# Kernel optimization log

Hardware: AMD Instinct MI355X
Metric: run time of the kernel (lower is better)

## Reference

```python
import jax, jax.numpy as jnp
import numpy as np

D_MODEL = 1024
HEAD_DIM = 256
MEMORY_SIZE = 64
SPARSITY_RATIO = 0.1
NEG_INF = -1.0e9


def setup_inputs() -> dict:
    key = jax.random.key(0)
    ks = jax.random.split(key, 16)
    s = lambda fan_in: 1.0 / np.sqrt(fan_in)
    inp = {
        "x": jax.random.normal(ks[0], (2, 4096, D_MODEL), dtype=jnp.float32),
        # local attention head (qkv fused, no bias); weights stored [in, out]
        "local_qkv_w": jax.random.uniform(ks[1], (D_MODEL, 3 * HEAD_DIM), minval=-s(D_MODEL), maxval=s(D_MODEL)),
        # sparse global head
        "sparse_qkv_w": jax.random.uniform(ks[2], (D_MODEL, 3 * HEAD_DIM), minval=-s(D_MODEL), maxval=s(D_MODEL)),
        # memory head
        "memory_bank": jax.random.normal(ks[3], (MEMORY_SIZE, HEAD_DIM), dtype=jnp.float32),
        "memory_proj_w": jax.random.uniform(ks[4], (D_MODEL, HEAD_DIM), minval=-s(D_MODEL), maxval=s(D_MODEL)),
        "mem_out_w": jax.random.uniform(ks[5], (2 * HEAD_DIM, HEAD_DIM), minval=-s(2 * HEAD_DIM), maxval=s(2 * HEAD_DIM)),
        "mem_out_b": jax.random.uniform(ks[6], (HEAD_DIM,), minval=-s(2 * HEAD_DIM), maxval=s(2 * HEAD_DIM)),
        # prediction head
        "pred_in_w": jax.random.uniform(ks[7], (D_MODEL, HEAD_DIM), minval=-s(D_MODEL), maxval=s(D_MODEL)),
        "pred_in_b": jax.random.uniform(ks[8], (HEAD_DIM,), minval=-s(D_MODEL), maxval=s(D_MODEL)),
        "pred1_w": jax.random.uniform(ks[9], (HEAD_DIM, 2 * HEAD_DIM), minval=-s(HEAD_DIM), maxval=s(HEAD_DIM)),
        "pred1_b": jax.random.uniform(ks[10], (2 * HEAD_DIM,), minval=-s(HEAD_DIM), maxval=s(HEAD_DIM)),
        "pred2_w": jax.random.uniform(ks[11], (2 * HEAD_DIM, HEAD_DIM), minval=-s(2 * HEAD_DIM), maxval=s(2 * HEAD_DIM)),
        "pred2_b": jax.random.uniform(ks[12], (HEAD_DIM,), minval=-s(2 * HEAD_DIM), maxval=s(2 * HEAD_DIM)),
        # warboss output projection
        "warboss_w": jax.random.uniform(ks[13], (4 * HEAD_DIM, D_MODEL), minval=-s(4 * HEAD_DIM), maxval=s(4 * HEAD_DIM)),
        "warboss_b": jax.random.uniform(ks[14], (D_MODEL,), minval=-s(4 * HEAD_DIM), maxval=s(4 * HEAD_DIM)),
    }
    return inp


def _full_attention(x, qkv_w, scale):
    # x: [B,S,D] -> q,k,v: [B,S,H]
    qkv = x @ qkv_w
    q, k, v = jnp.split(qkv, 3, axis=-1)
    scores = jnp.einsum("bsh,bth->bst", q, k) * scale  # [B,S,S]
    probs = jax.nn.softmax(scores, axis=-1)
    return probs @ v


def _sparse_global_attention(x, qkv_w, scale):
    qkv = x @ qkv_w
    q, k, v = jnp.split(qkv, 3, axis=-1)
    scores = jnp.einsum("bsh,bth->bst", q, k) * scale  # [B,S,S]
    seq_len = x.shape[1]
    k_sparse = max(1, int(seq_len * SPARSITY_RATIO))
    topk_vals, _ = jax.lax.top_k(scores, k_sparse)
    kth = topk_vals[..., -1:]  # [B,S,1] threshold
    masked = jnp.where(scores >= kth, scores, NEG_INF)
    probs = jax.nn.softmax(masked, axis=-1)
    return probs @ v


def _memory_head(x, memory_bank, memory_proj_w, mem_out_w, mem_out_b):
    x_proj = x @ memory_proj_w  # [B,S,H]
    mem_scores = jnp.einsum("bsh,mh->bsm", x_proj, memory_bank)
    mem_weights = jax.nn.softmax(mem_scores, axis=-1)
    retrieved = jnp.einsum("bsm,mh->bsh", mem_weights, memory_bank)
    combined = jnp.concatenate([x_proj, retrieved], axis=-1)
    return combined @ mem_out_w + mem_out_b


def _prediction_head(x, pred_in_w, pred_in_b, pred1_w, pred1_b, pred2_w, pred2_b):
    h = x @ pred_in_w + pred_in_b
    h = h @ pred1_w + pred1_b
    h = jax.nn.gelu(h, approximate=False)
    return h @ pred2_w + pred2_b


def reference(x, local_qkv_w, sparse_qkv_w, memory_bank, memory_proj_w, mem_out_w, mem_out_b, pred_in_w, pred_in_b, pred1_w, pred1_b, pred2_w, pred2_b, warboss_w, warboss_b):
    scale = HEAD_DIM ** -0.5
    local_out = _full_attention(x, local_qkv_w, scale)
    sparse_out = _sparse_global_attention(x, sparse_qkv_w, scale)
    mem_out = _memory_head(x, memory_bank, memory_proj_w, mem_out_w, mem_out_b)
    pred_out = _prediction_head(x, pred_in_w, pred_in_b, pred1_w, pred1_b, pred2_w, pred2_b)
    combined = jnp.concatenate([local_out, sparse_out, mem_out, pred_out], axis=-1)
    return combined @ warboss_w + warboss_b
```

## Files before the change

### kernel.cpp

```cpp
#include <hip/hip_runtime.h>
#include <hip/hip_bf16.h>

typedef __attribute__((ext_vector_type(8))) _Float16 half8;
typedef __attribute__((ext_vector_type(4))) _Float16 half4v;
typedef __attribute__((ext_vector_type(4))) float f32x4;

__device__ __forceinline__ float wred_max(float v){
  #pragma unroll
  for (int o = 32; o; o >>= 1) v = fmaxf(v, __shfl_xor(v, o));
  return v;
}
__device__ __forceinline__ float wred_sum(float v){
  #pragma unroll
  for (int o = 32; o; o >>= 1) v += __shfl_xor(v, o);
  return v;
}
__device__ __forceinline__ unsigned short h2u(_Float16 h){
  unsigned short u;
  __builtin_memcpy(&u, &h, 2);
  return u;
}
__device__ __forceinline__ float u2hf(unsigned short u){
  _Float16 h;
  __builtin_memcpy(&h, &u, 2);
  return (float)h;
}

#define GLOAD16(GP, LP) __builtin_amdgcn_global_load_lds( \
    (const __attribute__((address_space(1))) void*)(GP),  \
    (__attribute__((address_space(3))) void*)(LP), 16, 0, 0)

template<int BM, int BN, int OUT_F16, int ACT>
__global__ __launch_bounds__(256) void gemm_ht(
    const _Float16* __restrict__ A, long saz, int lda,
    const _Float16* __restrict__ B, long sbz, int ldb,
    void* __restrict__ Cv, long scz, int ldc,
    int K, float alpha, const float* __restrict__ bias)
{
  constexpr int FM = BM / 32, FN = BN / 32;
  __shared__ __align__(16) _Float16 Asl[2][BM * 32];
  __shared__ __align__(16) _Float16 Bsl[2][BN * 32];
  const int t = threadIdx.x;
  const int wid = t >> 6, lane = t & 63;
  const int wr = wid >> 1, wc = wid & 1;
  const int lr = lane & 15, kg = lane >> 4;
  A += (long)blockIdx.z * saz;
  B += (long)blockIdx.z * sbz;
  const long row0 = (long)blockIdx.y * BM;
  const long col0 = (long)blockIdx.x * BN;

  const int arow_t = t >> 2, acol_t = (t & 3) * 8;

  auto stage = [&](int buf, int k0){
    #pragma unroll
    for (int r = 0; r < BM / 64; r++){
      const _Float16* gp = A + (row0 + r*64 + arow_t) * (long)lda + k0 + acol_t;
      GLOAD16(gp, (char*)Asl[buf] + r*4096 + wid*1024);
    }
    #pragma unroll
    for (int r = 0; r < BN / 64; r++){
      const _Float16* gp = B + (col0 + r*64 + arow_t) * (long)ldb + k0 + acol_t;
      GLOAD16(gp, (char*)Bsl[buf] + r*4096 + wid*1024);
    }
  };

  f32x4 acc[FM][FN];
  #pragma unroll
  for (int i = 0; i < FM; i++)
    #pragma unroll
    for (int j = 0; j < FN; j++)
      acc[i][j] = (f32x4){0.f, 0.f, 0.f, 0.f};

  stage(0, 0);
  __syncthreads();
  int cur = 0;
  for (int k0 = 0; k0 < K; k0 += 32){
    if (k0 + 32 < K) stage(cur ^ 1, k0 + 32);
    half8 af[FM], bfv[FN];
    #pragma unroll
    for (int i = 0; i < FM; i++)
      af[i] = *(const half8*)((const char*)Asl[cur] + (wr*(BM/2) + i*16 + lr)*64 + kg*16);
    #pragma unroll
    for (int j = 0; j < FN; j++)
      bfv[j] = *(const half8*)((const char*)Bsl[cur] + (wc*(BN/2) + j*16 + lr)*64 + kg*16);
    #pragma unroll
    for (int i = 0; i < FM; i++)
      #pragma unroll
      for (int j = 0; j < FN; j++)
        acc[i][j] = __builtin_amdgcn_mfma_f32_16x16x32_f16(af[i], bfv[j], acc[i][j], 0, 0, 0);
    __syncthreads();
    cur ^= 1;
  }

  _Float16* Ch = (_Float16*)Cv + (long)blockIdx.z * scz;
  float*    Cf = (float*)Cv    + (long)blockIdx.z * scz;
  #pragma unroll
  for (int i = 0; i < FM; i++){
    #pragma unroll
    for (int j = 0; j < FN; j++){
      #pragma unroll
      for (int q = 0; q < 4; q++){
        long rr = row0 + wr*(BM/2) + i*16 + kg*4 + q;
        long cc = col0 + wc*(BN/2) + j*16 + lr;
        float val = acc[i][j][q] * alpha;
        if (bias) val += bias[cc];
        if constexpr (ACT) val = 0.5f * val * (1.0f + erff(val * 0.70710678118654752f));
        if constexpr (OUT_F16) Ch[rr*(long)ldc + cc] = (_Float16)val;
        else                   Cf[rr*(long)ldc + cc] = val;
      }
    }
  }
}

template<int BM, int BN, int SPARSE>
__global__ __launch_bounds__(256) void gemm_pv_exp(
    const _Float16* __restrict__ A, long saz, int lda,
    const _Float16* __restrict__ B, long sbz, int ldb,
    const float4* __restrict__ mlthr,
    _Float16* __restrict__ Ph, int nsplit, int Ksplit)
{
  constexpr int FM = BM / 32, FN = BN / 32;
  __shared__ __align__(16) _Float16 Asl[2][BM * 32];
  __shared__ __align__(16) _Float16 Bsl[2][BN * 32];
  const int t = threadIdx.x;
  const int wid = t >> 6, lane = t & 63;
  const int wr = wid >> 1, wc = wid & 1;
  const int lr = lane & 15, kg = lane >> 4;
  const int z = blockIdx.z, batch = z / nsplit, split = z % nsplit;
  A += (long)batch * saz;
  B += (long)batch * sbz;
  _Float16* Pz = Ph + (size_t)z * (4096 * 256);
  const long row0 = (long)blockIdx.y * BM;
  const int Kbase = split * Ksplit;

  const long arow = row0 + (t >> 2);
  const float4 mt = mlthr[(long)batch*4096 + arow];
  const float m = mt.x, thr = mt.z;
  const _Float16* Ap = A + arow * (long)lda + Kbase + (t & 3) * 8;

  const int arow_t = t >> 2, acol_t = (t & 3) * 8;

  auto stageB = [&](int buf, int k0){
    #pragma unroll
    for (int r = 0; r < BN / 64; r++){
      const _Float16* gp = B + (r*64 + arow_t) * (long)ldb + Kbase + k0 + acol_t;
      GLOAD16(gp, (char*)Bsl[buf] + r*4096 + wid*1024);
    }
  };
  auto expw = [&](int buf, half8 ld){
    half8 st;
    #pragma unroll
    for (int e = 0; e < 8; e++){
      float v = (float)ld[e];
      float ev;
      if constexpr (SPARSE) ev = (v >= thr) ? __expf(v - m) : 0.f;
      else                  ev = __expf(v - m);
      st[e] = (_Float16)ev;
    }
    *(half8*)((char*)Asl[buf] + t*16) = st;
  };

  f32x4 acc[FM][FN];
  #pragma unroll
  for (int i = 0; i < FM; i++)
    #pragma unroll
    for (int j = 0; j < FN; j++)
      acc[i][j] = (f32x4){0.f, 0.f, 0.f, 0.f};

  stageB(0, 0);
  expw(0, *(const half8*)(Ap + 0));
  __syncthreads();
  int cur = 0;
  for (int k0 = 0; k0 < Ksplit; k0 += 32){
    const bool more = (k0 + 32 < Ksplit);
    half8 lda_next;
    if (more){
      stageB(cur ^ 1, k0 + 32);
      lda_next = *(const half8*)(Ap + k0 + 32);
    }
    half8 af[FM], bfv[FN];
    #pragma unroll
    for (int i = 0; i < FM; i++)
      af[i] = *(const half8*)((const char*)Asl[cur] + (wr*(BM/2) + i*16 + lr)*64 + kg*16);
    #pragma unroll
    for (int j = 0; j < FN; j++)
      bfv[j] = *(const half8*)((const char*)Bsl[cur] + (wc*(BN/2) + j*16 + lr)*64 + kg*16);
    #pragma unroll
    for (int i = 0; i < FM; i++)
      #pragma unroll
      for (int j = 0; j < FN; j++)
        acc[i][j] = __builtin_amdgcn_mfma_f32_16x16x32_f16(af[i], bfv[j], acc[i][j], 0, 0, 0);
    if (more) expw(cur ^ 1, lda_next);
    __syncthreads();
    cur ^= 1;
  }

  #pragma unroll
  for (int i = 0; i < FM; i++)
    #pragma unroll
    for (int j = 0; j < FN; j++)
      #pragma unroll
      for (int q = 0; q < 4; q++){
        long rr = row0 + wr*(BM/2) + i*16 + kg*4 + q;
        long cc = wc*(BN/2) + j*16 + lr;
        Pz[rr*256 + cc] = (_Float16)acc[i][j][q];
      }
}

__global__ __launch_bounds__(256) void reduce8h(const _Float16* __restrict__ Ph,
                                                const float4* __restrict__ mlthr,
                                                _Float16* __restrict__ dst, int coff, int nq){
  int i = blockIdx.x * 256 + threadIdx.x;
  if (i >= nq) return;
  int b = i >> 18;
  int r = i & 262143;
  int row = r >> 6, col4 = r & 63;
  float sx = 0.f, sy = 0.f, sz = 0.f, sw = 0.f;
  #pragma unroll
  for (int sp = 0; sp < 8; sp++){
    half4v p = *(const half4v*)(Ph + (((size_t)(b*8 + sp)*4096 + row)*256 + col4*4));
    sx += (float)p[0]; sy += (float)p[1]; sz += (float)p[2]; sw += (float)p[3];
  }
  const float inv = 1.0f / mlthr[(long)b*4096 + row].y;
  half4v o;
  o[0] = (_Float16)(sx*inv); o[1] = (_Float16)(sy*inv);
  o[2] = (_Float16)(sz*inv); o[3] = (_Float16)(sw*inv);
  *(half4v*)(dst + ((size_t)b*4096 + row)*1024 + coff + col4*4) = o;
}

__global__ __launch_bounds__(256) void cast_xh(const float* __restrict__ in,
                                               _Float16* __restrict__ out, int n8){
  int i = blockIdx.x * 256 + threadIdx.x;
  const int stride = gridDim.x * 256;
  for (; i < n8; i += stride){
    float4 a = ((const float4*)in)[2*i];
    float4 b = ((const float4*)in)[2*i + 1];
    half8 o;
    o[0]=(_Float16)a.x; o[1]=(_Float16)a.y; o[2]=(_Float16)a.z; o[3]=(_Float16)a.w;
    o[4]=(_Float16)b.x; o[5]=(_Float16)b.y; o[6]=(_Float16)b.z; o[7]=(_Float16)b.w;
    *(half8*)(out + (size_t)i*8) = o;
  }
}

__global__ __launch_bounds__(256) void transpose_cast_w(const float* __restrict__ in, int R, int C,
                                                        _Float16* __restrict__ out){
  __shared__ float tile[32][33];
  const int c0 = blockIdx.x * 32, r0 = blockIdx.y * 32;
  const int tx = threadIdx.x & 31, ty = threadIdx.x >> 5;
  #pragma unroll
  for (int i = 0; i < 32; i += 8)
    tile[ty+i][tx] = in[(size_t)(r0+ty+i)*C + c0+tx];
  __syncthreads();
  #pragma unroll
  for (int i = 0; i < 32; i += 8)
    out[(size_t)(c0+ty+i)*R + r0+tx] = (_Float16)tile[tx][ty+i];
}

__global__ __launch_bounds__(256) void transpose_h(
    const _Float16* __restrict__ in, long in_z, int ld_in,
    _Float16* __restrict__ out, long out_z, int ld_out)
{
  __shared__ _Float16 tile[32][34];
  const _Float16* ip = in + (long)blockIdx.z * in_z;
  _Float16* op = out + (long)blockIdx.z * out_z;
  const int c0 = blockIdx.x * 32, r0 = blockIdx.y * 32;
  const int tx = threadIdx.x & 31, ty = threadIdx.x >> 5;
  #pragma unroll
  for (int i = 0; i < 32; i += 8)
    tile[ty+i][tx] = ip[(long)(r0+ty+i)*ld_in + c0+tx];
  __syncthreads();
  #pragma unroll
  for (int i = 0; i < 32; i += 8)
    op[(long)(c0+ty+i)*ld_out + r0+tx] = tile[tx][ty+i];
}

__global__ __launch_bounds__(256) void rowstat_local(const _Float16* __restrict__ sc,
                                                     float4* __restrict__ mlthr){
  __shared__ float red[4], red2[4];
  const int t = threadIdx.x, lane = t & 63, wid = t >> 6;
  const _Float16* p = sc + (size_t)blockIdx.x * 4096;
  half8 a = ((const half8*)p)[t*2];
  half8 b = ((const half8*)p)[t*2 + 1];
  float v[16];
  #pragma unroll
  for (int e = 0; e < 8; e++){ v[e] = (float)a[e]; v[8+e] = (float)b[e]; }
  float m = v[0];
  #pragma unroll
  for (int e = 1; e < 16; e++) m = fmaxf(m, v[e]);
  m = wred_max(m);
  if (lane == 0) red[wid] = m;
  __syncthreads();
  m = fmaxf(fmaxf(red[0], red[1]), fmaxf(red[2], red[3]));
  float s = 0.f;
  #pragma unroll
  for (int e = 0; e < 16; e++) s += __expf(v[e] - m);
  s = wred_sum(s);
  if (lane == 0) red2[wid] = s;
  __syncthreads();
  if (t == 0){
    s = red2[0] + red2[1] + red2[2] + red2[3];
    mlthr[blockIdx.x] = make_float4(m, s, -3.0e38f, 0.f);
  }
}

__global__ __launch_bounds__(256) void rowstat_sparse(const _Float16* __restrict__ sc,
                                                      float4* __restrict__ mlthr, int ksel){
  __shared__ unsigned hist4[4][256];
  __shared__ unsigned hrev[256];
  __shared__ unsigned suf[257];
  __shared__ unsigned wtot[4];
  __shared__ int selb;
  __shared__ float red[4], red2[4];
  const int t = threadIdx.x, lane = t & 63, wid = t >> 6;
  const _Float16* p = sc + (size_t)blockIdx.x * 4096;
  half8 a = ((const half8*)p)[t*2];
  half8 b = ((const half8*)p)[t*2 + 1];
  float v[16]; unsigned kk[16];
  #pragma unroll
  for (int e = 0; e < 8; e++){
    unsigned short u0 = h2u(a[e]);
    unsigned short u1 = h2u(b[e]);
    kk[e]   = (u0 & 0x8000u) ? (unsigned)(unsigned short)~u0 : (unsigned)(u0 | 0x8000u);
    kk[8+e] = (u1 & 0x8000u) ? (unsigned)(unsigned short)~u1 : (unsigned)(u1 | 0x8000u);
    v[e] = (float)a[e]; v[8+e] = (float)b[e];
  }
  float m = v[0];
  #pragma unroll
  for (int e = 1; e < 16; e++) m = fmaxf(m, v[e]);
  m = wred_max(m);
  if (lane == 0) red[wid] = m;
  __syncthreads();
  m = fmaxf(fmaxf(red[0], red[1]), fmaxf(red[2], red[3]));

  ((uint4*)hist4)[t] = (uint4){0u,0u,0u,0u};
  __syncthreads();
  #pragma unroll
  for (int e = 0; e < 16; e++) atomicAdd(&hist4[wid][kk[e] >> 8], 1u);
  __syncthreads();
  hrev[t] = hist4[0][t] + hist4[1][t] + hist4[2][t] + hist4[3][t];
  __syncthreads();
  unsigned x = hrev[255 - t];
  #pragma unroll
  for (int o = 1; o < 64; o <<= 1){
    unsigned y = __shfl_up(x, o);
    if (lane >= o) x += y;
  }
  if (lane == 63) wtot[wid] = x;
  __syncthreads();
  #pragma unroll
  for (int w = 0; w < 4; w++) if (w < wid) x += wtot[w];
  suf[255 - t] = x;
  if (t == 0) suf[256] = 0u;
  __syncthreads();
  const unsigned ku = (unsigned)ksel;
  if (suf[t] >= ku && suf[t+1] < ku) selb = t;
  __syncthreads();
  const int b1 = selb;
  const unsigned rem = ku - suf[b1+1];
  __syncthreads();

  ((uint4*)hist4)[t] = (uint4){0u,0u,0u,0u};
  __syncthreads();
  #pragma unroll
  for (int e = 0; e < 16; e++)
    if ((int)(kk[e] >> 8) == b1) atomicAdd(&hist4[wid][kk[e] & 255u], 1u);
  __syncthreads();
  hrev[t] = hist4[0][t] + hist4[1][t] + hist4[2][t] + hist4[3][t];
  __syncthreads();
  x = hrev[255 - t];
  #pragma unroll
  for (int o = 1; o < 64; o <<= 1){
    unsigned y = __shfl_up(x, o);
    if (lane >= o) x += y;
  }
  if (lane == 63) wtot[wid] = x;
  __syncthreads();
  #pragma unroll
  for (int w = 0; w < 4; w++) if (w < wid) x += wtot[w];
  suf[255 - t] = x;
  if (t == 0) suf[256] = 0u;
  __syncthreads();
  if (suf[t] >= rem && suf[t+1] < rem) selb = t;
  __syncthreads();
  const unsigned Tkey = ((unsigned)b1 << 8) | (unsigned)selb;
  const unsigned short tu = (Tkey & 0x8000u) ? (unsigned short)(Tkey & 0x7fffu)
                                             : (unsigned short)~Tkey;
  const float thr = u2hf(tu);

  float s = 0.f;
  #pragma unroll
  for (int e = 0; e < 16; e++)
    s += (v[e] >= thr) ? __expf(v[e] - m) : 0.f;
  s = wred_sum(s);
  if (lane == 0) red2[wid] = s;
  __syncthreads();
  if (t == 0){
    s = red2[0] + red2[1] + red2[2] + red2[3];
    mlthr[blockIdx.x] = make_float4(m, s, thr, 0.f);
  }
}

__global__ __launch_bounds__(256) void msoftmax64(const float* __restrict__ mscore,
                                                  _Float16* __restrict__ mprob){
  const int t = threadIdx.x, lane = t & 63, wid = t >> 6;
  const size_t row = (size_t)blockIdx.x * 4 + wid;
  float v = mscore[row*64 + lane];
  float m = wred_max(v);
  float e = expf(v - m);
  float s = wred_sum(e);
  mprob[row*64 + lane] = (_Float16)(e / s);
}

extern "C" void kernel_launch(void* const* d_in, const int* in_sizes, int n_in,
                              void* d_out, int out_size, void* d_ws, size_t ws_size,
                              hipStream_t stream)
{
  const float* x             = (const float*)d_in[0];
  const float* local_qkv_w   = (const float*)d_in[1];
  const float* sparse_qkv_w  = (const float*)d_in[2];
  const float* memory_bank   = (const float*)d_in[3];
  const float* memory_proj_w = (const float*)d_in[4];
  const float* mem_out_w     = (const float*)d_in[5];
  const float* mem_out_b     = (const float*)d_in[6];
  const float* pred_in_w     = (const float*)d_in[7];
  const float* pred_in_b     = (const float*)d_in[8];
  const float* pred1_w       = (const float*)d_in[9];
  const float* pred1_b       = (const float*)d_in[10];
  const float* pred2_w       = (const float*)d_in[11];
  const float* pred2_b       = (const float*)d_in[12];
  const float* warboss_w     = (const float*)d_in[13];
  const float* warboss_b     = (const float*)d_in[14];
  float* out = (float*)d_out;
  _Float16* Ph = (_Float16*)d_out;

  char* wsb = (char*)d_ws;
  _Float16*  scores_h = (_Float16*)wsb;
  _Float16*  x_h      = (_Float16*)wsb;
  _Float16*  mem_cat  = (_Float16*)(wsb + 16777216);
  _Float16*  h_in     = (_Float16*)(wsb + 25165824);
  _Float16*  h1       = (_Float16*)(wsb + 29360128);
  float*     mscore   = (float*)(wsb + 37748736);
  _Float16*  mprob    = (_Float16*)(wsb + 39845888);
  _Float16*  qkv_l    = (_Float16*)(wsb + 67108864);
  _Float16*  qkv_s    = (_Float16*)(wsb + 79691776);
  _Float16*  Vt       = (_Float16*)(wsb + 92274688);
  _Float16*  comb     = (_Float16*)(wsb + 96468992);
  _Float16*  lqkvT    = (_Float16*)(wsb + 113246208);
  _Float16*  sqkvT    = lqkvT  + 786432;
  _Float16*  mprojT   = sqkvT  + 786432;
  _Float16*  moutT    = mprojT + 262144;
  _Float16*  pinT     = moutT  + 131072;
  _Float16*  p1T      = pinT   + 262144;
  _Float16*  p2T      = p1T    + 131072;
  _Float16*  wbT      = p2T    + 131072;
  _Float16*  bank_h   = wbT    + 1048576;
  _Float16*  bankT_h  = bank_h + 16384;
  float4*    mlthr    = (float4*)(bankT_h + 16384);

  const dim3 blk(256);
  const float scale = 0.0625f;
  const long QZ  = (long)4096 * 768;
  const long VZ  = (long)256 * 4096;
  const long SZH = (long)4096 * 4096;

  cast_xh<<<dim3(2048), blk, 0, stream>>>(x, x_h, 1048576);
  cast_xh<<<dim3(8), blk, 0, stream>>>(memory_bank, bank_h, 2048);
  transpose_cast_w<<<dim3(24,32), blk, 0, stream>>>(local_qkv_w,  1024,  768, lqkvT);
  transpose_cast_w<<<dim3(24,32), blk, 0, stream>>>(sparse_qkv_w, 1024,  768, sqkvT);
  transpose_cast_w<<<dim3( 8,32), blk, 0, stream>>>(memory_proj_w,1024,  256, mprojT);
  transpose_cast_w<<<dim3( 8,16), blk, 0, stream>>>(mem_out_w,     512,  256, moutT);
  transpose_cast_w<<<dim3( 8,32), blk, 0, stream>>>(pred_in_w,    1024,  256, pinT);
  transpose_cast_w<<<dim3(16, 8), blk, 0, stream>>>(pred1_w,       256,  512, p1T);
  transpose_cast_w<<<dim3( 8,16), blk, 0, stream>>>(pred2_w,       512,  256, p2T);
  transpose_cast_w<<<dim3(32,32), blk, 0, stream>>>(warboss_w,    1024, 1024, wbT);
  transpose_cast_w<<<dim3( 8, 2), blk, 0, stream>>>(memory_bank,    64,  256, bankT_h);

  gemm_ht<128,128,1,0><<<dim3(6,64,2), blk, 0, stream>>>(x_h,0,1024, lqkvT,786432,1024,
                                                         qkv_l,6291456,768, 1024, 1.f, nullptr);

  gemm_ht<64,64,1,0><<<dim3(4,128), blk, 0, stream>>>(x_h,0,1024, mprojT,0,1024, mem_cat,0,512, 1024, 1.f, nullptr);
  gemm_ht<64,64,0,0><<<dim3(1,128), blk, 0, stream>>>(mem_cat,0,512, bank_h,0,256, (void*)mscore,0,64, 256, 1.f, nullptr);
  msoftmax64<<<dim3(2048), blk, 0, stream>>>(mscore, mprob);
  gemm_ht<64,64,1,0><<<dim3(4,128), blk, 0, stream>>>(mprob,0,64, bankT_h,0,64, mem_cat+256,0,512, 64, 1.f, nullptr);
  gemm_ht<64,64,1,0><<<dim3(4,128), blk, 0, stream>>>(mem_cat,0,512, moutT,0,512, comb+512,0,1024, 512, 1.f, mem_out_b);

  gemm_ht<64,64,1,0><<<dim3(4,128), blk, 0, stream>>>(x_h,0,1024, pinT,0,1024, h_in,0,256, 1024, 1.f, pred_in_b);
  gemm_ht<64,128,1,1><<<dim3(4,128), blk, 0, stream>>>(h_in,0,256, p1T,0,256, h1,0,512, 256, 1.f, pred1_b);
  gemm_ht<64,64,1,0><<<dim3(4,128), blk, 0, stream>>>(h1,0,512, p2T,0,512, comb+768,0,1024, 512, 1.f, pred2_b);

  transpose_h<<<dim3(8,128,2), blk, 0, stream>>>(qkv_l+512, QZ, 768, Vt, VZ, 4096);
  gemm_ht<128,128,1,0><<<dim3(32,32,2), blk, 0, stream>>>(qkv_l,QZ,768, qkv_l+256,QZ,768,
                                                          (void*)scores_h,SZH,4096, 256, scale, nullptr);
  rowstat_local<<<dim3(8192), blk, 0, stream>>>(scores_h, mlthr);
  gemm_pv_exp<64,256,0><<<dim3(1,64,16), blk, 0, stream>>>(scores_h,SZH,4096, Vt,VZ,4096, mlthr, Ph, 8, 512);
  reduce8h<<<dim3(2048), blk, 0, stream>>>(Ph, mlthr, comb, 0, 524288);

  transpose_h<<<dim3(8,128,2), blk, 0, stream>>>(qkv_s+512, QZ, 768, Vt, VZ, 4096);
  gemm_ht<128,128,1,0><<<dim3(32,32,2), blk, 0, stream>>>(qkv_s,QZ,768, qkv_s+256,QZ,768,
                                                          (void*)scores_h,SZH,4096, 256, scale, nullptr);
  rowstat_sparse<<<dim3(8192), blk, 0, stream>>>(scores_h, mlthr, 409);
  gemm_pv_exp<64,256,1><<<dim3(1,64,16), blk, 0, stream>>>(scores_h,SZH,4096, Vt,VZ,4096, mlthr, Ph, 8, 512);
  reduce8h<<<dim3(2048), blk, 0, stream>>>(Ph, mlthr, comb, 256, 524288);

  gemm_ht<128,128,0,0><<<dim3(8,64), blk, 0, stream>>>(comb,0,1024, wbT,0,1024, (void*)out,0,1024, 1024, 1.f, warboss_b);
}
```

Before: 398.7 us.

## Use half-precision exp in softmax-PV kernel and XCD-aware block swizzle

Computes the softmax exponentials and threshold compare in fp16 with hexp instead of converting to fp32 and using __expf, which is meant to cut conversion and transcendental cost in the PV producer loop. Also remaps workgroup indices so that consecutive tiles land on the same XCD, aiming for better L2 reuse across chiplets. The dense threshold sentinel changes to -60000 so it fits in fp16. Doing the exp in fp16 loses some accuracy in the subtraction and exponent, and the swizzle is skipped when the grid size is not a multiple of 8.

Measured after the change: 396.6 us. No clear change (-0.5%).

```diff
diff --git a/kernel.cpp b/kernel.cpp
--- a/kernel.cpp
+++ b/kernel.cpp
@@ -1,5 +1,6 @@
 #include <hip/hip_runtime.h>
 #include <hip/hip_bf16.h>
+#include <hip/hip_fp16.h>
 
 typedef __attribute__((ext_vector_type(8))) _Float16 half8;
 typedef __attribute__((ext_vector_type(4))) _Float16 half4v;
@@ -24,6 +25,26 @@
   _Float16 h;
   __builtin_memcpy(&h, &u, 2);
   return (float)h;
+}
+__device__ __forceinline__ _Float16 hexp16(_Float16 d){
+  __half hd, he;
+  __builtin_memcpy(&hd, &d, 2);
+  he = hexp(hd);
+  _Float16 r;
+  __builtin_memcpy(&r, &he, 2);
+  return r;
+}
+
+__device__ __forceinline__ void xcd_swz(int &bx, int &by, int &bz){
+  const int gx = gridDim.x, gy = gridDim.y, gz = gridDim.z;
+  const long nwg = (long)gx * gy * gz;
+  if ((nwg & 7) != 0) return;
+  long flat = bx + (long)gx * (by + (long)gy * bz);
+  const long cpx = nwg >> 3;
+  flat = (flat & 7) * cpx + (flat >> 3);
+  bx = (int)(flat % gx); flat /= gx;
+  by = (int)(flat % gy);
+  bz = (int)(flat / gy);
 }
 
 #define GLOAD16(GP, LP) __builtin_amdgcn_global_load_lds( \
@@ -44,10 +65,12 @@
   const int wid = t >> 6, lane = t & 63;
   const int wr = wid >> 1, wc = wid & 1;
   const int lr = lane & 15, kg = lane >> 4;
-  A += (long)blockIdx.z * saz;
-  B += (long)blockIdx.z * sbz;
-  const long row0 = (long)blockIdx.y * BM;
-  const long col0 = (long)blockIdx.x * BN;
+  int bx = blockIdx.x, by = blockIdx.y, bz = blockIdx.z;
+  xcd_swz(bx, by, bz);
+  A += (long)bz * saz;
+  B += (long)bz * sbz;
+  const long row0 = (long)by * BM;
+  const long col0 = (long)bx * BN;
 
   const int arow_t = t >> 2, acol_t = (t & 3) * 8;
 
@@ -92,8 +115,8 @@
     cur ^= 1;
   }
 
-  _Float16* Ch = (_Float16*)Cv + (long)blockIdx.z * scz;
-  float*    Cf = (float*)Cv    + (long)blockIdx.z * scz;
+  _Float16* Ch = (_Float16*)Cv + (long)bz * scz;
+  float*    Cf = (float*)Cv    + (long)bz * scz;
   #pragma unroll
   for (int i = 0; i < FM; i++){
     #pragma unroll
@@ -126,16 +149,19 @@
   const int wid = t >> 6, lane = t & 63;
   const int wr = wid >> 1, wc = wid & 1;
   const int lr = lane & 15, kg = lane >> 4;
-  const int z = blockIdx.z, batch = z / nsplit, split = z % nsplit;
+  int bx = blockIdx.x, by = blockIdx.y, bz = blockIdx.z;
+  xcd_swz(bx, by, bz);
+  const int z = bz, batch = z / nsplit, split = z % nsplit;
   A += (long)batch * saz;
   B += (long)batch * sbz;
   _Float16* Pz = Ph + (size_t)z * (4096 * 256);
-  const long row0 = (long)blockIdx.y * BM;
+  const long row0 = (long)by * BM;
   const int Kbase = split * Ksplit;
 
   const long arow = row0 + (t >> 2);
   const float4 mt = mlthr[(long)batch*4096 + arow];
-  const float m = mt.x, thr = mt.z;
+  const _Float16 mh  = (_Float16)mt.x;
+  const _Float16 thh = (_Float16)mt.z;
   const _Float16* Ap = A + arow * (long)lda + Kbase + (t & 3) * 8;
 
   const int arow_t = t >> 2, acol_t = (t & 3) * 8;
@@ -151,11 +177,9 @@
     half8 st;
     #pragma unroll
     for (int e = 0; e < 8; e++){
-      float v = (float)ld[e];
-      float ev;
-      if constexpr (SPARSE) ev = (v >= thr) ? __expf(v - m) : 0.f;
-      else                  ev = __expf(v - m);
-      st[e] = (_Float16)ev;
+      _Float16 ev = hexp16(ld[e] - mh);
+      if constexpr (SPARSE) st[e] = (ld[e] >= thh) ? ev : (_Float16)0.f;
+      else                  st[e] = ev;
     }
     *(half8*)((char*)Asl[buf] + t*16) = st;
   };
@@ -299,7 +323,7 @@
   __syncthreads();
   if (t == 0){
     s = red2[0] + red2[1] + red2[2] + red2[3];
-    mlthr[blockIdx.x] = make_float4(m, s, -3.0e38f, 0.f);
+    mlthr[blockIdx.x] = make_float4(m, s, -60000.0f, 0.f);
   }
 }
 
```
